# Optimization experiments

Measured on AMD Instinct MI355X. Metric: run time of the kernel, lower is better.

## Reference

```python
import jax, jax.numpy as jnp
import numpy as np

NODE_DIM = 256
EDGE_DIM = 64
TIME_DIM = 1024
HEADS = 8
HEAD_DIM = NODE_DIM // HEADS
MLP = 2
BS, N = 32, 48
BN = BS * N
E = BS * N * (N - 1)


def _lin(k, fin, fout):
    return jax.random.normal(k, (fin, fout), dtype=jnp.float32) / np.sqrt(fin)


def _edge_index():
    idx = np.arange(N)
    src, dst = np.meshgrid(idx, idx, indexing='ij')
    m = src != dst
    src, dst = src[m], dst[m]              # [N*(N-1)] per graph
    offs = (np.arange(BS) * N)[:, None]
    row = (offs + src[None, :]).reshape(-1)
    col = (offs + dst[None, :]).reshape(-1)
    return jnp.asarray(np.stack([row, col]), dtype=jnp.int32)


def setup_inputs() -> dict:
    key = jax.random.key(0)
    ks = jax.random.split(key, 32)
    d = {
        'pos': jax.random.normal(ks[0], (BN, 3), jnp.float32),
        'h': jax.random.normal(ks[1], (BN, NODE_DIM), jnp.float32),
        'edge_attr': jax.random.normal(ks[2], (E, EDGE_DIM), jnp.float32),
        'node_mask': jnp.ones((BN, 1), jnp.float32),
        'node_time_emb': jax.random.normal(ks[3], (BN, TIME_DIM), jnp.float32),
        'edge_time_emb': jax.random.normal(ks[4], (E, TIME_DIM), jnp.float32),
        'edge_index': _edge_index(),
        # edge_emb: Linear(edge_dim+1 -> edge_dim)
        'W_ee': _lin(ks[5], EDGE_DIM + 1, EDGE_DIM), 'b_ee': jnp.zeros((EDGE_DIM,)),
        # AdaLN time MLPs (SiLU -> Linear)
        'W_nt': _lin(ks[6], TIME_DIM, 6 * NODE_DIM), 'b_nt': jnp.zeros((6 * NODE_DIM,)),
        'W_et': _lin(ks[7], TIME_DIM, 6 * EDGE_DIM), 'b_et': jnp.zeros((6 * EDGE_DIM,)),
        # Trans_Layer sparse attention
        'Wq': _lin(ks[8], NODE_DIM, NODE_DIM), 'bq': jnp.zeros((NODE_DIM,)),
        'Wk': _lin(ks[9], NODE_DIM, NODE_DIM), 'bk': jnp.zeros((NODE_DIM,)),
        'Wv': _lin(ks[10], NODE_DIM, NODE_DIM), 'bv': jnp.zeros((NODE_DIM,)),
        'We0': _lin(ks[11], EDGE_DIM, NODE_DIM),
        'We1': _lin(ks[12], EDGE_DIM, NODE_DIM),
        'W_n2e': _lin(ks[13], NODE_DIM, EDGE_DIM), 'b_n2e': jnp.zeros((EDGE_DIM,)),
        # node FFN
        'W_ff1': _lin(ks[14], NODE_DIM, MLP * NODE_DIM), 'b_ff1': jnp.zeros((MLP * NODE_DIM,)),
        'W_ff2': _lin(ks[15], MLP * NODE_DIM, NODE_DIM), 'b_ff2': jnp.zeros((NODE_DIM,)),
        # edge FFN
        'W_ff3': _lin(ks[16], EDGE_DIM, MLP * EDGE_DIM), 'b_ff3': jnp.zeros((MLP * EDGE_DIM,)),
        'W_ff4': _lin(ks[17], MLP * EDGE_DIM, EDGE_DIM), 'b_ff4': jnp.zeros((EDGE_DIM,)),
        # CondEquiUpdate
        'coors_scale': jnp.full((1,), 0.01, jnp.float32),
        'W_ut': _lin(ks[18], TIME_DIM, 2 * NODE_DIM), 'b_ut': jnp.zeros((2 * NODE_DIM,)),
        'W_ui': _lin(ks[19], 2 * NODE_DIM + EDGE_DIM + 1, NODE_DIM), 'b_ui': jnp.zeros((NODE_DIM,)),
        'W_uc1': _lin(ks[20], NODE_DIM, NODE_DIM), 'b_uc1': jnp.zeros((NODE_DIM,)),
        'W_uc2': _lin(ks[21], NODE_DIM, 1),
    }
    return d


def _ln(x):  # LayerNorm, no affine, eps=1e-6
    m = x.mean(-1, keepdims=True)
    v = ((x - m) ** 2).mean(-1, keepdims=True)
    return (x - m) * jax.lax.rsqrt(v + 1e-6)


def _modulate(x, shift, scale):
    return x * (1 + scale) + shift


def _block(pos, h, edge_attr, node_mask, node_time_emb, edge_time_emb, edge_index,
           W_ee, b_ee, W_nt, b_nt, W_et, b_et, Wq, bq, Wk, bk, Wv, bv, We0, We1,
           W_n2e, b_n2e, W_ff1, b_ff1, W_ff2, b_ff2, W_ff3, b_ff3, W_ff4, b_ff4,
           coors_scale, W_ut, b_ut, W_ui, b_ui, W_uc1, b_uc1, W_uc2):
    row, col = edge_index[0], edge_index[1]  # row = source j, col = target i
    diff = pos[row] - pos[col]                              # [E,3]
    dist = jnp.sqrt(jnp.sum(diff * diff, -1, keepdims=True) + 1e-12)  # [E,1]
    ea = jnp.concatenate([dist, edge_attr], -1) @ W_ee + b_ee

    nt = jax.nn.silu(node_time_emb) @ W_nt + b_nt
    n_sh_msa, n_sc_msa, n_g_msa, n_sh_mlp, n_sc_mlp, n_g_mlp = jnp.split(nt, 6, axis=1)
    et = jax.nn.silu(edge_time_emb) @ W_et + b_et
    e_sh_msa, e_sc_msa, e_g_msa, e_sh_mlp, e_sc_mlp, e_g_mlp = jnp.split(et, 6, axis=1)

    hh = _modulate(_ln(h), n_sh_msa, n_sc_msa)
    ea = _modulate(_ln(ea), e_sh_msa, e_sc_msa)

    # sparse multi-head attention over edges (Trans_Layer)
    q = (hh @ Wq + bq).reshape(BN, HEADS, HEAD_DIM)
    k = (hh @ Wk + bk).reshape(BN, HEADS, HEAD_DIM)
    v = (hh @ Wv + bv).reshape(BN, HEADS, HEAD_DIM)
    e0 = (ea @ We0).reshape(E, HEADS, HEAD_DIM)
    e1 = (ea @ We1).reshape(E, HEADS, HEAD_DIM)
    alpha = jnp.sum(q[col] * k[row] * e0, -1) / np.sqrt(HEAD_DIM)  # [E,H]
    mx = jax.ops.segment_max(alpha, col, num_segments=BN)
    ex = jnp.exp(alpha - mx[col])
    den = jax.ops.segment_sum(ex, col, num_segments=BN)
    att = ex / (den[col] + 1e-16)
    msg = v[row] * e1 * att[:, :, None]
    h_node = jax.ops.segment_sum(msg, col, num_segments=BN).reshape(BN, NODE_DIM)

    h_edge = (h_node[row] + h_node[col]) @ W_n2e + b_n2e

    h_node = h + n_g_msa * h_node
    h_node = _modulate(_ln(h_node), n_sh_mlp, n_sc_mlp) * node_mask
    ff = jax.nn.silu(h_node @ W_ff1 + b_ff1) @ W_ff2 + b_ff2
    h_out = (h_node + n_g_mlp * ff) * node_mask

    h_e = edge_attr + e_g_msa * h_edge
    h_e = _modulate(_ln(h_e), e_sh_mlp, e_sc_mlp)
    ffe = jax.nn.silu(h_e @ W_ff3 + b_ff3) @ W_ff4 + b_ff4
    h_edge_out = h_e + e_g_mlp * ffe

    # CondEquiUpdate: equivariant coordinate update
    h_input = jnp.concatenate([h_out[row], h_out[col], h_edge_out, dist], -1)
    nrm = jnp.linalg.norm(diff, axis=-1, keepdims=True)
    cdiff = diff / jnp.clip(nrm, 1e-8) * coors_scale        # CoorsNorm(scale_init=0.01)
    t_shift, t_scale = jnp.split(jax.nn.silu(edge_time_emb) @ W_ut + b_ut, 2, axis=1)
    inv = _modulate(_ln(h_input @ W_ui + b_ui), t_shift, t_scale)
    inv = jnp.tanh(jax.nn.silu(inv @ W_uc1 + b_uc1) @ W_uc2)  # [E,1]
    trans = cdiff * inv
    pos_out = pos + jax.ops.segment_sum(trans, row, num_segments=BN)
    return h_out, h_edge_out, pos_out


def reference(pos, h, edge_attr, node_mask, node_time_emb, edge_time_emb, edge_index,
              W_ee, b_ee, W_nt, b_nt, W_et, b_et, Wq, bq, Wk, bk, Wv, bv, We0, We1,
              W_n2e, b_n2e, W_ff1, b_ff1, W_ff2, b_ff2, W_ff3, b_ff3, W_ff4, b_ff4,
              coors_scale, W_ut, b_ut, W_ui, b_ui, W_uc1, b_uc1, W_uc2):
    return _block(pos, h, edge_attr, node_mask, node_time_emb, edge_time_emb, edge_index,
                  W_ee, b_ee, W_nt, b_nt, W_et, b_et, Wq, bq, Wk, bk, Wv, bv, We0, We1,
                  W_n2e, b_n2e, W_ff1, b_ff1, W_ff2, b_ff2, W_ff3, b_ff3, W_ff4, b_ff4,
                  coors_scale, W_ut, b_ut, W_ui, b_ui, W_uc1, b_uc1, W_uc2)
```

## Files before the change

kernel.cpp:

```cpp
#include <hip/hip_runtime.h>

typedef unsigned short u16;
typedef __attribute__((ext_vector_type(4))) u16 u16x4;
typedef __attribute__((ext_vector_type(8))) u16 u16x8;
typedef __attribute__((ext_vector_type(8))) short s16x8;
typedef __attribute__((ext_vector_type(4))) float f32x4;

#define E_CNT 72192
#define BN_CNT 1536
#define EPG 2256

__device__ __forceinline__ float b2f(u16 u) {
    union { unsigned int i; float f; } x; x.i = ((unsigned int)u) << 16; return x.f;
}
__device__ __forceinline__ u16 f2b(float f) {
    union { float f; unsigned int i; } x; x.f = f;
    unsigned int r = x.i + 0x7fffu + ((x.i >> 16) & 1u);
    return (u16)(r >> 16);
}
__device__ __forceinline__ float siluf(float x) { return x / (1.f + expf(-x)); }

__device__ __forceinline__ void gll16(const void* g, void* l) {
    __builtin_amdgcn_global_load_lds(
        (const __attribute__((address_space(1))) void*)g,
        (__attribute__((address_space(3))) void*)l, 16, 0, 0);
}

__device__ __forceinline__ float wave_ln64(float x) {
    float s = x;
    #pragma unroll
    for (int off = 1; off < 64; off <<= 1) s += __shfl_xor(s, off);
    float mean = s * 0.015625f;
    float d = x - mean;
    float v2 = d * d;
    #pragma unroll
    for (int off = 1; off < 64; off <<= 1) v2 += __shfl_xor(v2, off);
    return d * rsqrtf(v2 * 0.015625f + 1e-6f);
}

__device__ __forceinline__ float block_ln256(float x) {
    __shared__ float tmp[4];
    int t = threadIdx.x;
    float s = x;
    #pragma unroll
    for (int off = 1; off < 64; off <<= 1) s += __shfl_xor(s, off);
    if ((t & 63) == 0) tmp[t >> 6] = s;
    __syncthreads();
    float mean = (tmp[0] + tmp[1] + tmp[2] + tmp[3]) * (1.f / 256.f);
    float d = x - mean;
    float v2 = d * d;
    #pragma unroll
    for (int off = 1; off < 64; off <<= 1) v2 += __shfl_xor(v2, off);
    __syncthreads();
    if ((t & 63) == 0) tmp[t >> 6] = v2;
    __syncthreads();
    float var = (tmp[0] + tmp[1] + tmp[2] + tmp[3]) * (1.f / 256.f);
    return d * rsqrtf(var + 1e-6f);
}

template<int ACT, int OUTBF>
__global__ __launch_bounds__(256) void k_gemm(
    const u16* __restrict__ A, const u16* __restrict__ Bt,
    const float* __restrict__ bias, void* __restrict__ C,
    int M, int N, int K)
{
    __shared__ u16 As[64][40];
    __shared__ u16 Bs[64][40];
    int bn0 = blockIdx.x * 64, bm0 = blockIdx.y * 64;
    int t = threadIdx.x;
    int lane = t & 63, wave = t >> 6;
    int wm = wave >> 1, wn = wave & 1;
    int lr = t >> 2, lc = (t & 3) * 8;
    f32x4 acc[2][2] = {};
    const u16* Ap = A + (size_t)(bm0 + lr) * K + lc;
    const u16* Bp = Bt + (size_t)(bn0 + lr) * K + lc;
    int fr = lane & 15, fk = (lane >> 4) * 8;
    for (int k0 = 0; k0 < K; k0 += 32) {
        *(u16x8*)&As[lr][lc] = *(const u16x8*)(Ap + k0);
        *(u16x8*)&Bs[lr][lc] = *(const u16x8*)(Bp + k0);
        __syncthreads();
        s16x8 a0 = *(const s16x8*)&As[wm * 32 + fr][fk];
        s16x8 a1 = *(const s16x8*)&As[wm * 32 + 16 + fr][fk];
        s16x8 b0 = *(const s16x8*)&Bs[wn * 32 + fr][fk];
        s16x8 b1 = *(const s16x8*)&Bs[wn * 32 + 16 + fr][fk];
        acc[0][0] = __builtin_amdgcn_mfma_f32_16x16x32_bf16(a0, b0, acc[0][0], 0, 0, 0);
        acc[0][1] = __builtin_amdgcn_mfma_f32_16x16x32_bf16(a0, b1, acc[0][1], 0, 0, 0);
        acc[1][0] = __builtin_amdgcn_mfma_f32_16x16x32_bf16(a1, b0, acc[1][0], 0, 0, 0);
        acc[1][1] = __builtin_amdgcn_mfma_f32_16x16x32_bf16(a1, b1, acc[1][1], 0, 0, 0);
        __syncthreads();
    }
    int cIn = lane & 15, r4 = (lane >> 4) * 4;
    #pragma unroll
    for (int i = 0; i < 2; i++)
    #pragma unroll
    for (int j = 0; j < 2; j++) {
        int col = bn0 + wn * 32 + j * 16 + cIn;
        float bv = bias ? bias[col] : 0.f;
        #pragma unroll
        for (int r = 0; r < 4; r++) {
            int rowg = bm0 + wm * 32 + i * 16 + r4 + r;
            float vv = acc[i][j][r] + bv;
            if (ACT == 1) vv = siluf(vv);
            if (OUTBF) ((u16*)C)[(size_t)rowg * N + col] = f2b(vv);
            else       ((float*)C)[(size_t)rowg * N + col] = vv;
        }
    }
}

__global__ __launch_bounds__(256) void k_gemm_ff2ho(
    const u16* __restrict__ A, const u16* __restrict__ Bt,
    const float* __restrict__ bias, const float* __restrict__ hmod,
    const float* __restrict__ nt, const float* __restrict__ mask,
    float* __restrict__ out, u16* __restrict__ hout_bf, int M, int N, int K)
{
    __shared__ u16 As[64][40];
    __shared__ u16 Bs[64][40];
    int bn0 = blockIdx.x * 64, bm0 = blockIdx.y * 64;
    int t = threadIdx.x;
    int lane = t & 63, wave = t >> 6;
    int wm = wave >> 1, wn = wave & 1;
    int lr = t >> 2, lc = (t & 3) * 8;
    f32x4 acc[2][2] = {};
    const u16* Ap = A + (size_t)(bm0 + lr) * K + lc;
    const u16* Bp = Bt + (size_t)(bn0 + lr) * K + lc;
    int fr = lane & 15, fk = (lane >> 4) * 8;
    for (int k0 = 0; k0 < K; k0 += 32) {
        *(u16x8*)&As[lr][lc] = *(const u16x8*)(Ap + k0);
        *(u16x8*)&Bs[lr][lc] = *(const u16x8*)(Bp + k0);
        __syncthreads();
        s16x8 a0 = *(const s16x8*)&As[wm * 32 + fr][fk];
        s16x8 a1 = *(const s16x8*)&As[wm * 32 + 16 + fr][fk];
        s16x8 b0 = *(const s16x8*)&Bs[wn * 32 + fr][fk];
        s16x8 b1 = *(const s16x8*)&Bs[wn * 32 + 16 + fr][fk];
        acc[0][0] = __builtin_amdgcn_mfma_f32_16x16x32_bf16(a0, b0, acc[0][0], 0, 0, 0);
        acc[0][1] = __builtin_amdgcn_mfma_f32_16x16x32_bf16(a0, b1, acc[0][1], 0, 0, 0);
        acc[1][0] = __builtin_amdgcn_mfma_f32_16x16x32_bf16(a1, b0, acc[1][0], 0, 0, 0);
        acc[1][1] = __builtin_amdgcn_mfma_f32_16x16x32_bf16(a1, b1, acc[1][1], 0, 0, 0);
        __syncthreads();
    }
    int cIn = lane & 15, r4 = (lane >> 4) * 4;
    #pragma unroll
    for (int i = 0; i < 2; i++)
    #pragma unroll
    for (int j = 0; j < 2; j++) {
        int col = bn0 + wn * 32 + j * 16 + cIn;
        float bv = bias[col];
        #pragma unroll
        for (int r = 0; r < 4; r++) {
            int rowg = bm0 + wm * 32 + i * 16 + r4 + r;
            float x = acc[i][j][r] + bv;
            float v = (hmod[(size_t)rowg * 256 + col]
                     + nt[(size_t)rowg * 1536 + 1280 + col] * x) * mask[rowg];
            out[(size_t)rowg * 256 + col] = v;
            hout_bf[(size_t)rowg * 256 + col] = f2b(v);
        }
    }
}

__global__ __launch_bounds__(256) void k_gemm_ff4eo(
    const u16* __restrict__ A, const u16* __restrict__ Bt,
    const float* __restrict__ bias, const float* __restrict__ hemod,
    const u16* __restrict__ etf,
    float* __restrict__ out2, u16* __restrict__ heout_bf, int M, int N, int K)
{
    __shared__ u16 As[64][40];
    __shared__ u16 Bs[64][40];
    int bn0 = blockIdx.x * 64, bm0 = blockIdx.y * 64;
    int t = threadIdx.x;
    int lane = t & 63, wave = t >> 6;
    int wm = wave >> 1, wn = wave & 1;
    int lr = t >> 2, lc = (t & 3) * 8;
    f32x4 acc[2][2] = {};
    const u16* Ap = A + (size_t)(bm0 + lr) * K + lc;
    const u16* Bp = Bt + (size_t)(bn0 + lr) * K + lc;
    int fr = lane & 15, fk = (lane >> 4) * 8;
    for (int k0 = 0; k0 < K; k0 += 32) {
        *(u16x8*)&As[lr][lc] = *(const u16x8*)(Ap + k0);
        *(u16x8*)&Bs[lr][lc] = *(const u16x8*)(Bp + k0);
        __syncthreads();
        s16x8 a0 = *(const s16x8*)&As[wm * 32 + fr][fk];
        s16x8 a1 = *(const s16x8*)&As[wm * 32 + 16 + fr][fk];
        s16x8 b0 = *(const s16x8*)&Bs[wn * 32 + fr][fk];
        s16x8 b1 = *(const s16x8*)&Bs[wn * 32 + 16 + fr][fk];
        acc[0][0] = __builtin_amdgcn_mfma_f32_16x16x32_bf16(a0, b0, acc[0][0], 0, 0, 0);
        acc[0][1] = __builtin_amdgcn_mfma_f32_16x16x32_bf16(a0, b1, acc[0][1], 0, 0, 0);
        acc[1][0] = __builtin_amdgcn_mfma_f32_16x16x32_bf16(a1, b0, acc[1][0], 0, 0, 0);
        acc[1][1] = __builtin_amdgcn_mfma_f32_16x16x32_bf16(a1, b1, acc[1][1], 0, 0, 0);
        __syncthreads();
    }
    int cIn = lane & 15, r4 = (lane >> 4) * 4;
    #pragma unroll
    for (int i = 0; i < 2; i++)
    #pragma unroll
    for (int j = 0; j < 2; j++) {
        int col = bn0 + wn * 32 + j * 16 + cIn;
        float bv = bias[col];
        #pragma unroll
        for (int r = 0; r < 4; r++) {
            int rowg = bm0 + wm * 32 + i * 16 + r4 + r;
            float x = acc[i][j][r] + bv;
            float v = hemod[(size_t)rowg * 64 + col]
                    + b2f(etf[(size_t)rowg * 896 + 320 + col]) * x;
            out2[(size_t)rowg * 64 + col] = v;
            heout_bf[(size_t)rowg * 64 + col] = f2b(v);
        }
    }
}

template<int ACT, int OUTBF>
__global__ __launch_bounds__(256) void k_gemm128(
    const u16* __restrict__ A, const u16* __restrict__ Bt,
    const float* __restrict__ bias, void* __restrict__ C,
    int M, int N, int K)
{
    __shared__ u16 As[3][128 * 32];
    __shared__ u16 Bs[3][128 * 32];
    const int t = threadIdx.x;
    const int lane = t & 63, wv = t >> 6;
    const int wm = wv >> 1, wn = wv & 1;
    const int nwg = gridDim.x * gridDim.y;
    const int orig = blockIdx.y * gridDim.x + blockIdx.x;
    const int q8 = nwg >> 3, r8 = nwg & 7;
    const int xcd = orig & 7, lin = orig >> 3;
    const int wgid = (xcd < r8 ? xcd * (q8 + 1) : r8 * (q8 + 1) + (xcd - r8) * q8) + lin;
    const int bxs = wgid % gridDim.x, bys = wgid / gridDim.x;
    const int bn0 = bxs * 128, bm0 = bys * 128;
    const int srow = t >> 2;
    const int scol = ((t & 3) ^ ((t >> 3) & 3)) * 8;
    const u16* Ap = A + (size_t)(bm0 + srow) * K + scol;
    const u16* Bp = Bt + (size_t)(bn0 + srow) * K + scol;
    const size_t rstep = (size_t)64 * K;
    const int woff = wv * 16 * 32;
    const int fr = lane & 15;
    const int fkc = (((lane >> 4) ^ ((fr >> 1) & 3)) * 8);
    f32x4 acc[4][4] = {};
    const int NT = K >> 5;

    auto STAGE = [&](int b, int ko) {
        gll16(Ap + ko, &As[b][woff]);
        gll16(Ap + ko + rstep, &As[b][woff + 64 * 32]);
        gll16(Bp + ko, &Bs[b][woff]);
        gll16(Bp + ko + rstep, &Bs[b][woff + 64 * 32]);
    };
    auto COMPUTE = [&](int b) {
        const u16* aBase = &As[b][wm * 64 * 32];
        const u16* bBase = &Bs[b][wn * 64 * 32];
        s16x8 af[4], bfr[4];
        #pragma unroll
        for (int m = 0; m < 4; m++) af[m] = *(const s16x8*)&aBase[(m * 16 + fr) * 32 + fkc];
        #pragma unroll
        for (int n = 0; n < 4; n++) bfr[n] = *(const s16x8*)&bBase[(n * 16 + fr) * 32 + fkc];
        #pragma unroll
        for (int m = 0; m < 4; m++)
        #pragma unroll
        for (int n = 0; n < 4; n++)
            acc[m][n] = __builtin_amdgcn_mfma_f32_16x16x32_bf16(af[m], bfr[n], acc[m][n], 0, 0, 0);
    };

    STAGE(0, 0);
    if (NT > 1) STAGE(1, 32);
    int cur = 0;
    for (int tt = 0; tt < NT; tt++) {
        if (tt + 2 < NT) STAGE((cur + 2) % 3, (tt + 2) * 32);
        __builtin_amdgcn_sched_barrier(0);
        int ahead = NT - 1 - tt; if (ahead > 2) ahead = 2;
        if (ahead == 2)      asm volatile("s_waitcnt vmcnt(8)" ::: "memory");
        else if (ahead == 1) asm volatile("s_waitcnt vmcnt(4)" ::: "memory");
        else                 asm volatile("s_waitcnt vmcnt(0)" ::: "memory");
        __builtin_amdgcn_sched_barrier(0);
        __builtin_amdgcn_s_barrier();
        COMPUTE(cur);
        __builtin_amdgcn_s_barrier();
        __builtin_amdgcn_sched_barrier(0);
        cur = (cur + 1) % 3;
    }

    const int cIn = lane & 15, r4 = (lane >> 4) * 4;
    #pragma unroll
    for (int n = 0; n < 4; n++) {
        int col = bn0 + wn * 64 + n * 16 + cIn;
        float bv = bias ? bias[col] : 0.f;
        #pragma unroll
        for (int m = 0; m < 4; m++) {
            #pragma unroll
            for (int r = 0; r < 4; r++) {
                int rowg = bm0 + wm * 64 + m * 16 + r4 + r;
                float vv = acc[m][n][r] + bv;
                if (ACT == 1) vv = siluf(vv);
                if (OUTBF) ((u16*)C)[(size_t)rowg * N + col] = f2b(vv);
                else       ((float*)C)[(size_t)rowg * N + col] = vv;
            }
        }
    }
}

struct ConvJob { const float* W; u16* Wt; int ldw, k0, n0, K, tile_start, tiles_k; };
struct CopyJob { const float* src; float* dst; int n; };
struct BatchArgs { ConvJob cj[17]; CopyJob cp[5]; int conv_blocks; };

__global__ __launch_bounds__(256) void k_prep(BatchArgs a)
{
    __shared__ float ls[64][65];
    int b = blockIdx.x;
    int t = threadIdx.x;
    if (b < a.conv_blocks) {
        int j = 0;
        #pragma unroll 1
        while (j + 1 < 17 && a.cj[j + 1].tile_start <= b) ++j;
        const ConvJob J = a.cj[j];
        int local = b - J.tile_start;
        int tk = local % J.tiles_k, tn = local / J.tiles_k;
        int k0 = tk * 64, n0 = tn * 64;
        int cn = t & 63, rk = t >> 6;
        #pragma unroll
        for (int p = 0; p < 16; p++) {
            int kk = p * 4 + rk;
            ls[kk][cn] = J.W[(size_t)(J.k0 + k0 + kk) * J.ldw + J.n0 + n0 + cn];
        }
        __syncthreads();
        int ck = t & 63, rn = t >> 6;
        #pragma unroll
        for (int p = 0; p < 16; p++) {
            int nn = p * 4 + rn;
            J.Wt[(size_t)(n0 + nn) * J.K + k0 + ck] = f2b(ls[ck][nn]);
        }
    } else {
        int c = b - a.conv_blocks;
        const CopyJob C = a.cp[c];
        for (int i = t; i < C.n; i += 256) C.dst[i] = C.src[i];
    }
}

__global__ void k_silu_bf(const float* __restrict__ in, u16* __restrict__ out, int n4)
{
    int i = blockIdx.x * 256 + threadIdx.x;
    int stride = gridDim.x * 256;
    for (; i < n4; i += stride) {
        f32x4 v = *(const f32x4*)(in + (size_t)i * 4);
        u16x4 o;
        #pragma unroll
        for (int j = 0; j < 4; j++) o[j] = f2b(siluf(v[j]));
        *(u16x4*)(out + (size_t)i * 4) = o;
    }
}

__global__ __launch_bounds__(256) void k_edge_pre(
    const float* __restrict__ pos, const float* __restrict__ edge_attr,
    const int* __restrict__ ei, const float* __restrict__ W_ee,
    const float* __restrict__ b_ee, const float* __restrict__ coors_scale,
    const u16* __restrict__ etf,
    u16* __restrict__ ea_mod, float* __restrict__ dist, float* __restrict__ cdiff)
{
    __shared__ float Ws[65][64];
    int t = threadIdx.x;
    for (int i = t; i < 65 * 64; i += 256) Ws[i >> 6][i & 63] = W_ee[i];
    __syncthreads();
    int l = t & 63;
    float bee = b_ee[l];
    float cscale = coors_scale[0];
    for (int g = 0; g < 16; g++) {
        int e = blockIdx.x * 64 + g * 4 + (t >> 6);
        int row = ei[e], col = ei[E_CNT + e];
        float d0 = pos[row * 3 + 0] - pos[col * 3 + 0];
        float d1 = pos[row * 3 + 1] - pos[col * 3 + 1];
        float d2 = pos[row * 3 + 2] - pos[col * 3 + 2];
        float ssq = d0 * d0 + d1 * d1 + d2 * d2;
        float dst = sqrtf(ssq + 1e-12f);
        float nrm = sqrtf(ssq);
        float cs = cscale / fmaxf(nrm, 1e-8f);
        if (l == 0) {
            dist[e] = dst;
            cdiff[e * 3 + 0] = d0 * cs; cdiff[e * 3 + 1] = d1 * cs; cdiff[e * 3 + 2] = d2 * cs;
        }
        float attr = edge_attr[(size_t)e * 64 + l];
        float acc = dst * Ws[0][l];
        for (int f = 0; f < 64; f++) acc += __shfl(attr, f) * Ws[1 + f][l];
        acc += bee;
        float y = wave_ln64(acc);
        const u16* ep = etf + (size_t)e * 896;
        float m = y * (1.f + b2f(ep[64 + l])) + b2f(ep[l]);
        ea_mod[(size_t)e * 64 + l] = f2b(m);
    }
}

__global__ __launch_bounds__(256) void k_node_hh(
    const float* __restrict__ h, const float* __restrict__ nt, u16* __restrict__ hh)
{
    int n = blockIdx.x, c = threadIdx.x;
    float x = h[(size_t)n * 256 + c];
    float y = block_ln256(x);
    float m = y * (1.f + nt[(size_t)n * 1536 + 256 + c]) + nt[(size_t)n * 1536 + c];
    hh[(size_t)n * 256 + c] = f2b(m);
}

__global__ __launch_bounds__(256) void k_agg(
    const float* __restrict__ qkv, const u16* __restrict__ e01,
    float* __restrict__ hnode, u16* __restrict__ hnode_bf)
{
    int n = blockIdx.x;
    int b = n / 48, i = n % 48;
    int t = threadIdx.x;
    __shared__ float qs[8][33];
    __shared__ float att[47][8];
    __shared__ float mxs[8], dens[8];
    __shared__ int elist[47], slist[47];
    qs[t >> 5][t & 31] = qkv[(size_t)n * 768 + t];
    if (t < 47) {
        int s = t + (t >= i ? 1 : 0);
        slist[t] = s;
        elist[t] = b * EPG + s * 47 + (i < s ? i : i - 1);
    }
    __syncthreads();
    for (int idx = t; idx < 376; idx += 256) {
        int j = idx >> 3, hh = idx & 7;
        int src = b * 48 + slist[j];
        int e = elist[j];
        const float* kp = qkv + (size_t)src * 768 + 256 + hh * 32;
        const u16* ep = e01 + (size_t)e * 512 + hh * 32;
        float p = 0.f;
        #pragma unroll
        for (int d = 0; d < 32; d++) p += qs[hh][d] * kp[d] * b2f(ep[d]);
        att[j][hh] = p * 0.17677669529663687f;
    }
    __syncthreads();
    if (t < 8) {
        float m = -1e30f;
        for (int j = 0; j < 47; j++) m = fmaxf(m, att[j][t]);
        float den = 0.f;
        for (int j = 0; j < 47; j++) den += expf(att[j][t] - m);
        mxs[t] = m; dens[t] = den + 1e-16f;
    }
    __syncthreads();
    for (int idx = t; idx < 376; idx += 256) {
        int j = idx >> 3, hh = idx & 7;
        att[j][hh] = expf(att[j][hh] - mxs[hh]) / dens[hh];
    }
    __syncthreads();
    int c = t, hh = t >> 5;
    float acc = 0.f;
    for (int j = 0; j < 47; j++) {
        int src = b * 48 + slist[j];
        int e = elist[j];
        acc += att[j][hh] * qkv[(size_t)src * 768 + 512 + c] * b2f(e01[(size_t)e * 512 + 256 + c]);
    }
    hnode[(size_t)n * 256 + c] = acc;
    hnode_bf[(size_t)n * 256 + c] = f2b(acc);
}

__global__ __launch_bounds__(256) void k_node_mod(
    const float* __restrict__ h, const float* __restrict__ hnode_raw,
    const float* __restrict__ nt, const float* __restrict__ mask,
    float* __restrict__ hmod, u16* __restrict__ hmod_bf)
{
    int n = blockIdx.x, c = threadIdx.x;
    float x = h[(size_t)n * 256 + c] + nt[(size_t)n * 1536 + 512 + c] * hnode_raw[(size_t)n * 256 + c];
    float y = block_ln256(x);
    float m = (y * (1.f + nt[(size_t)n * 1536 + 1024 + c]) + nt[(size_t)n * 1536 + 768 + c]) * mask[n];
    hmod[(size_t)n * 256 + c] = m;
    hmod_bf[(size_t)n * 256 + c] = f2b(m);
}

__global__ __launch_bounds__(256) void k_edge_mod(
    const float* __restrict__ Q1, const float* __restrict__ b_n2e,
    const float* __restrict__ edge_attr, const int* __restrict__ ei,
    const u16* __restrict__ etf, float* __restrict__ hemod, u16* __restrict__ hemod_bf)
{
    int e = blockIdx.x * 4 + (threadIdx.x >> 6);
    int l = threadIdx.x & 63;
    int row = ei[e], col = ei[E_CNT + e];
    float hedge = Q1[(size_t)row * 64 + l] + Q1[(size_t)col * 64 + l] + b_n2e[l];
    const u16* ep = etf + (size_t)e * 896;
    float x = edge_attr[(size_t)e * 64 + l] + b2f(ep[128 + l]) * hedge;
    float y = wave_ln64(x);
    float m = y * (1.f + b2f(ep[256 + l])) + b2f(ep[192 + l]);
    hemod[(size_t)e * 64 + l] = m;
    hemod_bf[(size_t)e * 64 + l] = f2b(m);
}

__global__ __launch_bounds__(256) void k_inv_pre(
    const float* __restrict__ p12,
    const u16* __restrict__ P3, const float* __restrict__ dist,
    const float* __restrict__ W_ui, const float* __restrict__ b_ui,
    const int* __restrict__ ei, const u16* __restrict__ etf, u16* __restrict__ invmod)
{
    int e = blockIdx.x, c = threadIdx.x;
    int row = ei[e], col = ei[E_CNT + e];
    float x = p12[(size_t)row * 512 + c] + p12[(size_t)col * 512 + 256 + c]
            + b2f(P3[(size_t)e * 256 + c]) + dist[e] * W_ui[576 * 256 + c] + b_ui[c];
    float y = block_ln256(x);
    const u16* ep = etf + (size_t)e * 896;
    float m = y * (1.f + b2f(ep[640 + c])) + b2f(ep[384 + c]);
    invmod[(size_t)e * 256 + c] = f2b(m);
}

__global__ __launch_bounds__(256) void k_inv(const u16* __restrict__ uc1,
                                             const float* __restrict__ W_uc2,
                                             float* __restrict__ inv)
{
    int e = blockIdx.x * 4 + (threadIdx.x >> 6);
    int l = threadIdx.x & 63;
    u16x4 v = *(const u16x4*)(uc1 + (size_t)e * 256 + l * 4);
    const float* w = W_uc2 + l * 4;
    float s = b2f(v[0]) * w[0] + b2f(v[1]) * w[1] + b2f(v[2]) * w[2] + b2f(v[3]) * w[3];
    #pragma unroll
    for (int off = 1; off < 64; off <<= 1) s += __shfl_xor(s, off);
    if (l == 0) inv[e] = tanhf(s);
}

__global__ void k_pos(const float* __restrict__ pos, const float* __restrict__ cdiff,
                      const float* __restrict__ inv, float* __restrict__ out3)
{
    int n = blockIdx.x * 256 + threadIdx.x;
    if (n >= BN_CNT) return;
    int b = n / 48, s = n % 48;
    int e0 = b * EPG + s * 47;
    float a0 = 0.f, a1 = 0.f, a2 = 0.f;
    for (int j = 0; j < 47; j++) {
        float f = inv[e0 + j];
        a0 += cdiff[(size_t)(e0 + j) * 3 + 0] * f;
        a1 += cdiff[(size_t)(e0 + j) * 3 + 1] * f;
        a2 += cdiff[(size_t)(e0 + j) * 3 + 2] * f;
    }
    out3[n * 3 + 0] = pos[n * 3 + 0] + a0;
    out3[n * 3 + 1] = pos[n * 3 + 1] + a1;
    out3[n * 3 + 2] = pos[n * 3 + 2] + a2;
}

extern "C" void kernel_launch(void* const* d_in, const int* in_sizes, int n_in,
                              void* d_out, int out_size, void* d_ws, size_t ws_size,
                              hipStream_t stream)
{
    (void)in_sizes; (void)n_in; (void)out_size; (void)ws_size;
    const float* pos       = (const float*)d_in[0];
    const float* h         = (const float*)d_in[1];
    const float* edge_attr = (const float*)d_in[2];
    const float* node_mask = (const float*)d_in[3];
    const float* nte       = (const float*)d_in[4];
    const float* ete       = (const float*)d_in[5];
    const int*   ei        = (const int*)d_in[6];
    const float* W_ee = (const float*)d_in[7];  const float* b_ee = (const float*)d_in[8];
    const float* W_nt = (const float*)d_in[9];  const float* b_nt = (const float*)d_in[10];
    const float* W_et = (const float*)d_in[11]; const float* b_et = (const float*)d_in[12];
    const float* Wq  = (const float*)d_in[13];  const float* bq  = (const float*)d_in[14];
    const float* Wk  = (const float*)d_in[15];  const float* bk  = (const float*)d_in[16];
    const float* Wv  = (const float*)d_in[17];  const float* bv  = (const float*)d_in[18];
    const float* We0 = (const float*)d_in[19];  const float* We1 = (const float*)d_in[20];
    const float* W_n2e = (const float*)d_in[21]; const float* b_n2e = (const float*)d_in[22];
    const float* W_ff1 = (const float*)d_in[23]; const float* b_ff1 = (const float*)d_in[24];
    const float* W_ff2 = (const float*)d_in[25]; const float* b_ff2 = (const float*)d_in[26];
    const float* W_ff3 = (const float*)d_in[27]; const float* b_ff3 = (const float*)d_in[28];
    const float* W_ff4 = (const float*)d_in[29]; const float* b_ff4 = (const float*)d_in[30];
    const float* coors_scale = (const float*)d_in[31];
    const float* W_ut = (const float*)d_in[32]; const float* b_ut = (const float*)d_in[33];
    const float* W_ui = (const float*)d_in[34]; const float* b_ui = (const float*)d_in[35];
    const float* W_uc1 = (const float*)d_in[36]; const float* b_uc1 = (const float*)d_in[37];
    const float* W_uc2 = (const float*)d_in[38];

    const size_t E = E_CNT;
    char* ws = (char*)d_ws;
    size_t off = 0;
    auto AL = [&](size_t b) { size_t o = off; off += (b + 255) & ~(size_t)255; return o; };

    size_t o_wtcat  = AL(896 * 1024 * 2);
    size_t o_wtnt   = AL(1536 * 1024 * 2);
    size_t o_wtqkv  = AL(768 * 256 * 2);
    size_t o_wte01  = AL(512 * 64 * 2);
    size_t o_wtn2e  = AL(64 * 256 * 2);
    size_t o_wtff1  = AL(512 * 256 * 2), o_wtff2 = AL(256 * 512 * 2);
    size_t o_wtff3  = AL(128 * 64 * 2),  o_wtff4 = AL(64 * 128 * 2);
    size_t o_wtuiab = AL(512 * 256 * 2);
    size_t o_wtuic  = AL(256 * 64 * 2),  o_wtuc1 = AL(256 * 256 * 2);
    size_t o_bias896 = AL(896 * 4);
    size_t o_bias768 = AL(768 * 4);
    size_t o_reg1 = AL(E * 1024 * 2);
    size_t o_etf  = AL(E * 896 * 2);
    size_t o_ntes = AL(1536 * 1024 * 2);
    size_t o_ntf  = AL((size_t)1536 * 1536 * 4);
    size_t o_eamod = AL(E * 64 * 2);
    size_t o_dist = AL(E * 4), o_cdiff = AL(E * 12);
    size_t o_qkv  = AL(1536 * 768 * 4);
    size_t o_reg3 = AL(E * 512 * 2);
    size_t o_hnode = AL(1536 * 256 * 4), o_hnodebf = AL(1536 * 256 * 2);
    size_t o_q1 = AL(1536 * 64 * 4);
    size_t o_hh = AL(1536 * 256 * 2);
    size_t o_hmod = AL(1536 * 256 * 4), o_hmodbf = AL(1536 * 256 * 2);
    size_t o_ff1 = AL(1536 * 512 * 2);
    size_t o_houtbf = AL(1536 * 256 * 2);
    size_t o_hemod = AL(E * 64 * 4), o_hemodbf = AL(E * 64 * 2);
    size_t o_p12 = AL(1536 * 512 * 4);
    size_t o_inv = AL(E * 4);
    size_t o_etes = o_reg1;
    size_t o_p3 = o_reg1;
    size_t o_invmod = o_reg1 + E * 256 * 2;
    size_t o_uc1o = o_reg1 + E * 256 * 4;
    size_t o_e01 = o_reg3;
    size_t o_ffem = o_reg3;
    size_t o_heoutbf = o_reg3 + E * 128 * 2 + E * 64 * 4;

    #define WSU(o) ((u16*)(ws + (o)))
    #define WSF(o) ((float*)(ws + (o)))

    {
        BatchArgs a;
        int s = 0; int j = 0;
        auto add = [&](const float* W, u16* Wt, int ldw, int k0, int n0, int K, int NC) {
            a.cj[j++] = ConvJob{W, Wt, ldw, k0, n0, K, s, K / 64};
            s += (K / 64) * (NC / 64);
        };
        add(W_et, WSU(o_wtcat), 384, 0, 0, 1024, 384);
        add(W_ut, WSU(o_wtcat) + (size_t)384 * 1024, 512, 0, 0, 1024, 512);
        add(W_nt, WSU(o_wtnt), 1536, 0, 0, 1024, 1536);
        add(Wq, WSU(o_wtqkv), 256, 0, 0, 256, 256);
        add(Wk, WSU(o_wtqkv) + (size_t)256 * 256, 256, 0, 0, 256, 256);
        add(Wv, WSU(o_wtqkv) + (size_t)512 * 256, 256, 0, 0, 256, 256);
        add(We0, WSU(o_wte01), 256, 0, 0, 64, 256);
        add(We1, WSU(o_wte01) + (size_t)256 * 64, 256, 0, 0, 64, 256);
        add(W_n2e, WSU(o_wtn2e), 64, 0, 0, 256, 64);
        add(W_ff1, WSU(o_wtff1), 512, 0, 0, 256, 512);
        add(W_ff2, WSU(o_wtff2), 256, 0, 0, 512, 256);
        add(W_ff3, WSU(o_wtff3), 128, 0, 0, 64, 128);
        add(W_ff4, WSU(o_wtff4), 64, 0, 0, 128, 64);
        add(W_ui, WSU(o_wtuiab), 256, 0, 0, 256, 256);
        add(W_ui, WSU(o_wtuiab) + (size_t)256 * 256, 256, 256, 0, 256, 256);
        add(W_ui, WSU(o_wtuic), 256, 512, 0, 64, 256);
        add(W_uc1, WSU(o_wtuc1), 256, 0, 0, 256, 256);
        a.conv_blocks = s;
        a.cp[0] = CopyJob{b_et, WSF(o_bias896), 384};
        a.cp[1] = CopyJob{b_ut, WSF(o_bias896) + 384, 512};
        a.cp[2] = CopyJob{bq, WSF(o_bias768), 256};
        a.cp[3] = CopyJob{bk, WSF(o_bias768) + 256, 256};
        a.cp[4] = CopyJob{bv, WSF(o_bias768) + 512, 256};
        k_prep<<<s + 5, 256, 0, stream>>>(a);
    }

    k_silu_bf<<<2048, 256, 0, stream>>>(ete, WSU(o_etes), (int)(E * 1024 / 4));
    k_silu_bf<<<1024, 256, 0, stream>>>(nte, WSU(o_ntes), 1536 * 1024 / 4);

    k_gemm128<0, 1><<<dim3(7, 564), 256, 0, stream>>>(WSU(o_etes), WSU(o_wtcat), WSF(o_bias896), WSU(o_etf), E_CNT, 896, 1024);
    k_gemm128<0, 0><<<dim3(12, 12), 256, 0, stream>>>(WSU(o_ntes), WSU(o_wtnt), b_nt, WSF(o_ntf), 1536, 1536, 1024);

    k_edge_pre<<<1128, 256, 0, stream>>>(pos, edge_attr, ei, W_ee, b_ee, coors_scale,
                                         WSU(o_etf), WSU(o_eamod), WSF(o_dist), WSF(o_cdiff));

    k_node_hh<<<1536, 256, 0, stream>>>(h, WSF(o_ntf), WSU(o_hh));
    k_gemm128<0, 0><<<dim3(6, 12), 256, 0, stream>>>(WSU(o_hh), WSU(o_wtqkv), WSF(o_bias768), WSF(o_qkv), 1536, 768, 256);
    k_gemm128<0, 1><<<dim3(4, 564), 256, 0, stream>>>(WSU(o_eamod), WSU(o_wte01), nullptr, WSU(o_e01), E_CNT, 512, 64);
    k_agg<<<1536, 256, 0, stream>>>(WSF(o_qkv), WSU(o_e01), WSF(o_hnode), WSU(o_hnodebf));

    k_gemm<0, 0><<<dim3(1, 24), 256, 0, stream>>>(WSU(o_hnodebf), WSU(o_wtn2e), nullptr, WSF(o_q1), 1536, 64, 256);

    k_node_mod<<<1536, 256, 0, stream>>>(h, WSF(o_hnode), WSF(o_ntf), node_mask, WSF(o_hmod), WSU(o_hmodbf));
    k_gemm128<1, 1><<<dim3(4, 12), 256, 0, stream>>>(WSU(o_hmodbf), WSU(o_wtff1), b_ff1, WSU(o_ff1), 1536, 512, 256);
    k_gemm_ff2ho<<<dim3(4, 24), 256, 0, stream>>>(WSU(o_ff1), WSU(o_wtff2), b_ff2,
                                                  WSF(o_hmod), WSF(o_ntf), node_mask,
                                                  (float*)d_out, WSU(o_houtbf), 1536, 256, 512);

    k_edge_mod<<<18048, 256, 0, stream>>>(WSF(o_q1), b_n2e, edge_attr, ei, WSU(o_etf), WSF(o_hemod), WSU(o_hemodbf));
    k_gemm128<1, 1><<<dim3(1, 564), 256, 0, stream>>>(WSU(o_hemodbf), WSU(o_wtff3), b_ff3, WSU(o_ffem), E_CNT, 128, 64);
    k_gemm_ff4eo<<<dim3(1, 1128), 256, 0, stream>>>(WSU(o_ffem), WSU(o_wtff4), b_ff4,
                                                    WSF(o_hemod), WSU(o_etf),
                                                    (float*)d_out + 393216, WSU(o_heoutbf), E_CNT, 64, 128);

    k_gemm128<0, 0><<<dim3(4, 12), 256, 0, stream>>>(WSU(o_houtbf), WSU(o_wtuiab), nullptr, WSF(o_p12), 1536, 512, 256);
    k_gemm128<0, 1><<<dim3(2, 564), 256, 0, stream>>>(WSU(o_heoutbf), WSU(o_wtuic), nullptr, WSU(o_p3), E_CNT, 256, 64);
    k_inv_pre<<<E_CNT, 256, 0, stream>>>(WSF(o_p12), WSU(o_p3), WSF(o_dist),
                                         W_ui, b_ui, ei, WSU(o_etf), WSU(o_invmod));
    k_gemm128<1, 1><<<dim3(2, 564), 256, 0, stream>>>(WSU(o_invmod), WSU(o_wtuc1), b_uc1, WSU(o_uc1o), E_CNT, 256, 256);
    k_inv<<<18048, 256, 0, stream>>>(WSU(o_uc1o), W_uc2, WSF(o_inv));
    k_pos<<<6, 256, 0, stream>>>(pos, WSF(o_cdiff), WSF(o_inv), (float*)d_out + 393216 + E_CNT * 64);

    #undef WSU
    #undef WSF
}
```

Before: 744.9 us.

## Merge independent edge and node GEMM pairs into single dual-job launches

Adds a k_gemm128_dual kernel that takes two GEMM job descriptors and splits the grid between them, so an edge-sized GEMM and a small node-sized GEMM run in one launch. Four such pairs are merged, and k_edge_mod is moved earlier so ff3 can pair with ff1. This removes launch gaps and lets the small node GEMMs fill the tail of the large edge GEMMs. In exchange, activation, output type and bias handling become runtime flags rather than template parameters, which may add some epilogue overhead or register pressure.

```diff
diff --git a/kernel.cpp b/kernel.cpp
--- a/kernel.cpp
+++ b/kernel.cpp
@@ -289,6 +289,96 @@
                 if (ACT == 1) vv = siluf(vv);
                 if (OUTBF) ((u16*)C)[(size_t)rowg * N + col] = f2b(vv);
                 else       ((float*)C)[(size_t)rowg * N + col] = vv;
+            }
+        }
+    }
+}
+
+struct GJob {
+    const u16* A; const u16* Bt; const float* bias; void* C;
+    int M, N, K, gx, nwg, act, outbf;
+};
+
+__global__ __launch_bounds__(256) void k_gemm128_dual(GJob ja, GJob jb)
+{
+    const bool first = (int)blockIdx.x < ja.nwg;
+    const GJob J = first ? ja : jb;
+    const int orig = first ? blockIdx.x : blockIdx.x - ja.nwg;
+    __shared__ u16 As[3][128 * 32];
+    __shared__ u16 Bs[3][128 * 32];
+    const int t = threadIdx.x;
+    const int lane = t & 63, wv = t >> 6;
+    const int wm = wv >> 1, wn = wv & 1;
+    const int K = J.K;
+    const int q8 = J.nwg >> 3, r8 = J.nwg & 7;
+    const int xcd = orig & 7, lin = orig >> 3;
+    const int wgid = (xcd < r8 ? xcd * (q8 + 1) : r8 * (q8 + 1) + (xcd - r8) * q8) + lin;
+    const int bxs = wgid % J.gx, bys = wgid / J.gx;
+    const int bn0 = bxs * 128, bm0 = bys * 128;
+    const int srow = t >> 2;
+    const int scol = ((t & 3) ^ ((t >> 3) & 3)) * 8;
+    const u16* Ap = J.A + (size_t)(bm0 + srow) * K + scol;
+    const u16* Bp = J.Bt + (size_t)(bn0 + srow) * K + scol;
+    const size_t rstep = (size_t)64 * K;
+    const int woff = wv * 16 * 32;
+    const int fr = lane & 15;
+    const int fkc = (((lane >> 4) ^ ((fr >> 1) & 3)) * 8);
+    f32x4 acc[4][4] = {};
+    const int NT = K >> 5;
+
+    auto STAGE = [&](int b, int ko) {
+        gll16(Ap + ko, &As[b][woff]);
+        gll16(Ap + ko + rstep, &As[b][woff + 64 * 32]);
+        gll16(Bp + ko, &Bs[b][woff]);
+        gll16(Bp + ko + rstep, &Bs[b][woff + 64 * 32]);
+    };
+    auto COMPUTE = [&](int b) {
+        const u16* aBase = &As[b][wm * 64 * 32];
+        const u16* bBase = &Bs[b][wn * 64 * 32];
+        s16x8 af[4], bfr[4];
+        #pragma unroll
+        for (int m = 0; m < 4; m++) af[m] = *(const s16x8*)&aBase[(m * 16 + fr) * 32 + fkc];
+        #pragma unroll
+        for (int n = 0; n < 4; n++) bfr[n] = *(const s16x8*)&bBase[(n * 16 + fr) * 32 + fkc];
+        #pragma unroll
+        for (int m = 0; m < 4; m++)
+        #pragma unroll
+        for (int n = 0; n < 4; n++)
+            acc[m][n] = __builtin_amdgcn_mfma_f32_16x16x32_bf16(af[m], bfr[n], acc[m][n], 0, 0, 0);
+    };
+
+    STAGE(0, 0);
+    if (NT > 1) STAGE(1, 32);
+    int cur = 0;
+    for (int tt = 0; tt < NT; tt++) {
+        if (tt + 2 < NT) STAGE((cur + 2) % 3, (tt + 2) * 32);
+        __builtin_amdgcn_sched_barrier(0);
+        int ahead = NT - 1 - tt; if (ahead > 2) ahead = 2;
+        if (ahead == 2)      asm volatile("s_waitcnt vmcnt(8)" ::: "memory");
+        else if (ahead == 1) asm volatile("s_waitcnt vmcnt(4)" ::: "memory");
+        else                 asm volatile("s_waitcnt vmcnt(0)" ::: "memory");
+        __builtin_amdgcn_sched_barrier(0);
+        __builtin_amdgcn_s_barrier();
+        COMPUTE(cur);
+        __builtin_amdgcn_s_barrier();
+        __builtin_amdgcn_sched_barrier(0);
+        cur = (cur + 1) % 3;
+    }
+
+    const int cIn = lane & 15, r4 = (lane >> 4) * 4;
+    #pragma unroll
+    for (int n = 0; n < 4; n++) {
+        int col = bn0 + wn * 64 + n * 16 + cIn;
+        float bv = J.bias ? J.bias[col] : 0.f;
+        #pragma unroll
+        for (int m = 0; m < 4; m++) {
+            #pragma unroll
+            for (int r = 0; r < 4; r++) {
+                int rowg = bm0 + wm * 64 + m * 16 + r4 + r;
+                float vv = acc[m][n][r] + bv;
+                if (J.act) vv = siluf(vv);
+                if (J.outbf) ((u16*)J.C)[(size_t)rowg * J.N + col] = f2b(vv);
+                else         ((float*)J.C)[(size_t)rowg * J.N + col] = vv;
             }
         }
     }
@@ -636,33 +726,54 @@
     k_silu_bf<<<2048, 256, 0, stream>>>(ete, WSU(o_etes), (int)(E * 1024 / 4));
     k_silu_bf<<<1024, 256, 0, stream>>>(nte, WSU(o_ntes), 1536 * 1024 / 4);
 
-    k_gemm128<0, 1><<<dim3(7, 564), 256, 0, stream>>>(WSU(o_etes), WSU(o_wtcat), WSF(o_bias896), WSU(o_etf), E_CNT, 896, 1024);
-    k_gemm128<0, 0><<<dim3(12, 12), 256, 0, stream>>>(WSU(o_ntes), WSU(o_wtnt), b_nt, WSF(o_ntf), 1536, 1536, 1024);
+    {
+        GJob ja{WSU(o_etes), WSU(o_wtcat), WSF(o_bias896), WSU(o_etf),
+                E_CNT, 896, 1024, 7, 3948, 0, 1};
+        GJob jb{WSU(o_ntes), WSU(o_wtnt), b_nt, WSF(o_ntf),
+                1536, 1536, 1024, 12, 144, 0, 0};
+        k_gemm128_dual<<<3948 + 144, 256, 0, stream>>>(ja, jb);
+    }
 
     k_edge_pre<<<1128, 256, 0, stream>>>(pos, edge_attr, ei, W_ee, b_ee, coors_scale,
                                          WSU(o_etf), WSU(o_eamod), WSF(o_dist), WSF(o_cdiff));
-
     k_node_hh<<<1536, 256, 0, stream>>>(h, WSF(o_ntf), WSU(o_hh));
-    k_gemm128<0, 0><<<dim3(6, 12), 256, 0, stream>>>(WSU(o_hh), WSU(o_wtqkv), WSF(o_bias768), WSF(o_qkv), 1536, 768, 256);
-    k_gemm128<0, 1><<<dim3(4, 564), 256, 0, stream>>>(WSU(o_eamod), WSU(o_wte01), nullptr, WSU(o_e01), E_CNT, 512, 64);
+
+    {
+        GJob ja{WSU(o_eamod), WSU(o_wte01), nullptr, WSU(o_e01),
+                E_CNT, 512, 64, 4, 2256, 0, 1};
+        GJob jb{WSU(o_hh), WSU(o_wtqkv), WSF(o_bias768), WSF(o_qkv),
+                1536, 768, 256, 6, 72, 0, 0};
+        k_gemm128_dual<<<2256 + 72, 256, 0, stream>>>(ja, jb);
+    }
     k_agg<<<1536, 256, 0, stream>>>(WSF(o_qkv), WSU(o_e01), WSF(o_hnode), WSU(o_hnodebf));
 
     k_gemm<0, 0><<<dim3(1, 24), 256, 0, stream>>>(WSU(o_hnodebf), WSU(o_wtn2e), nullptr, WSF(o_q1), 1536, 64, 256);
 
     k_node_mod<<<1536, 256, 0, stream>>>(h, WSF(o_hnode), WSF(o_ntf), node_mask, WSF(o_hmod), WSU(o_hmodbf));
-    k_gemm128<1, 1><<<dim3(4, 12), 256, 0, stream>>>(WSU(o_hmodbf), WSU(o_wtff1), b_ff1, WSU(o_ff1), 1536, 512, 256);
+    k_edge_mod<<<18048, 256, 0, stream>>>(WSF(o_q1), b_n2e, edge_attr, ei, WSU(o_etf), WSF(o_hemod), WSU(o_hemodbf));
+
+    {
+        GJob ja{WSU(o_hemodbf), WSU(o_wtff3), b_ff3, WSU(o_ffem),
+                E_CNT, 128, 64, 1, 564, 1, 1};
+        GJob jb{WSU(o_hmodbf), WSU(o_wtff1), b_ff1, WSU(o_ff1),
+                1536, 512, 256, 4, 48, 1, 1};
+        k_gemm128_dual<<<564 + 48, 256, 0, stream>>>(ja, jb);
+    }
+
     k_gemm_ff2ho<<<dim3(4, 24), 256, 0, stream>>>(WSU(o_ff1), WSU(o_wtff2), b_ff2,
                                                   WSF(o_hmod), WSF(o_ntf), node_mask,
                                                   (float*)d_out, WSU(o_houtbf), 1536, 256, 512);
-
-    k_edge_mod<<<18048, 256, 0, stream>>>(WSF(o_q1), b_n2e, edge_attr, ei, WSU(o_etf), WSF(o_hemod), WSU(o_hemodbf));
-    k_gemm128<1, 1><<<dim3(1, 564), 256, 0, stream>>>(WSU(o_hemodbf), WSU(o_wtff3), b_ff3, WSU(o_ffem), E_CNT, 128, 64);
     k_gemm_ff4eo<<<dim3(1, 1128), 256, 0, stream>>>(WSU(o_ffem), WSU(o_wtff4), b_ff4,
                                                     WSF(o_hemod), WSU(o_etf),
                                                     (float*)d_out + 393216, WSU(o_heoutbf), E_CNT, 64, 128);
 
-    k_gemm128<0, 0><<<dim3(4, 12), 256, 0, stream>>>(WSU(o_houtbf), WSU(o_wtuiab), nullptr, WSF(o_p12), 1536, 512, 256);
-    k_gemm128<0, 1><<<dim3(2, 564), 256, 0, stream>>>(WSU(o_heoutbf), WSU(o_wtuic), nullptr, WSU(o_p3), E_CNT, 256, 64);
+    {
+        GJob ja{WSU(o_heoutbf), WSU(o_wtuic), nullptr, WSU(o_p3),
+                E_CNT, 256, 64, 2, 1128, 0, 1};
+        GJob jb{WSU(o_houtbf), WSU(o_wtuiab), nullptr, WSF(o_p12),
+                1536, 512, 256, 4, 48, 0, 0};
+        k_gemm128_dual<<<1128 + 48, 256, 0, stream>>>(ja, jb);
+    }
     k_inv_pre<<<E_CNT, 256, 0, stream>>>(WSF(o_p12), WSU(o_p3), WSF(o_dist),
                                          W_ui, b_ui, ei, WSU(o_etf), WSU(o_invmod));
     k_gemm128<1, 1><<<dim3(2, 564), 256, 0, stream>>>(WSU(o_invmod), WSU(o_wtuc1), b_uc1, WSU(o_uc1o), E_CNT, 256, 256);
```

New measurement: 736.8 us. No clear change (-1.1%).
